# Kernel tuning notes

Hardware: AMD Instinct MI355X
Metric: run time of the kernel (lower is better)

Reference implementation:

```python
import jax, jax.numpy as jnp
import numpy as np

N, C, EMB_ROWS = 524288, 128, 32
SLOPE = 0.2  # leaky_relu negative slope


def setup_inputs() -> dict:
    key = jax.random.key(0)
    k1, k2, k3, k4, k5 = jax.random.split(key, 5)
    x = jax.random.normal(k1, (N, C), jnp.float32)
    perm = jax.random.permutation(k2, N)  # fixed stand-in for torch.randperm
    depth = jax.random.normal(k3, (EMB_ROWS, 128), jnp.float32)  # Embedding(32,128), N(0,1) init
    fan_in = 2 * C * 2
    bound = 1.0 / np.sqrt(fan_in)
    W = jax.random.uniform(k4, (C, 2 * C, 2), jnp.float32, -bound, bound)  # Conv1d weight (O,I,K)
    b = jax.random.uniform(k5, (C,), jnp.float32, -bound, bound)
    return {"x": x, "depth": depth, "W": W, "b": b, "perm": perm}


def reference(x, depth, W, b, perm):
    c = W.shape[0]
    x = x[perm]                      # random shuffle of rows
    x = x.T.reshape(1, c, -1)        # [1, C, N]
    i = 0
    # Python while over STATIC shapes -> unrolled at trace time (~log2(N) steps)
    while x.shape[-1] > 1:
        L = x.shape[-1]
        e = jnp.broadcast_to(depth[i].reshape(1, 128, 1), (1, 128, L))
        x = jnp.concatenate([x, e], axis=1)   # [1, 2C, L]
        x = jax.lax.conv_general_dilated(
            x, W, window_strides=(1,), padding="VALID",
            dimension_numbers=("NCH", "OIH", "NCH"))  # [1, C, L-1]
        x = x + b.reshape(1, -1, 1)
        x = jnp.where(x >= 0, x, SLOPE * x)   # leaky_relu(0.2)
        if x.shape[-1] == 1:
            break
        # MaxPool1d(2,2): floor(L/2), drops trailing element for odd L
        x = jax.lax.reduce_window(
            x, -jnp.inf, jax.lax.max,
            window_dimensions=(1, 1, 2), window_strides=(1, 1, 2),
            padding="VALID")
        i += 1
    return x.reshape(c, 1).T  # [1, C]
```

## Files before the change

kernel.cpp:

```cpp
#include <hip/hip_runtime.h>
#include <hip/hip_bf16.h>


typedef __bf16 v8bf __attribute__((ext_vector_type(8)));
typedef float v16f __attribute__((ext_vector_type(16)));

__device__ __forceinline__ ushort f2bf(float f) {
    __hip_bfloat16 h = __float2bfloat16(f);
    return *reinterpret_cast<ushort*>(&h);
}
__device__ __forceinline__ unsigned pack2(float lo, float hi) {
    return (unsigned)f2bf(lo) | ((unsigned)f2bf(hi) << 16);
}
__device__ __forceinline__ float leaky(float y) { return (y >= 0.f) ? y : 0.2f * y; }

#define ZACC {0.f,0.f,0.f,0.f,0.f,0.f,0.f,0.f,0.f,0.f,0.f,0.f,0.f,0.f,0.f,0.f}

__global__ void bias_kernel(const float* __restrict__ W, const float* __restrict__ b,
                            const float* __restrict__ depth, float* __restrict__ Bst) {
    int i = blockIdx.x, o = threadIdx.x;
    const float* Wo = W + (size_t)o * 512 + 256;
    const float* di = depth + (size_t)i * 128;
    float s = b[o];
#pragma unroll 8
    for (int c = 0; c < 128; ++c) s += di[c] * (Wo[2 * c] + Wo[2 * c + 1]);
    Bst[i * 128 + o] = s;
}

__global__ void repack_kernel(const float* __restrict__ W, ushort* __restrict__ A) {
    int o = blockIdx.x, c = threadIdx.x;
    float v = (c < 128) ? W[(size_t)o * 512 + 2 * c] : W[(size_t)o * 512 + 2 * (c - 128) + 1];
    A[o * 256 + c] = f2bf(v);
}

#define WAVE_SETUP()                                                          \
    const int tid = threadIdx.x;                                              \
    const int lane = tid & 63;                                                \
    const int w = tid >> 6;                                                   \
    const int n31 = lane & 31;                                                \
    const int h = lane >> 5;                                                  \
    v8bf af[16];                                                              \
    {                                                                         \
        const ushort* Arow = A + (size_t)(w * 32 + n31) * 256 + h * 8;        \
        _Pragma("unroll")                                                     \
        for (int s = 0; s < 16; ++s) af[s] = *(const v8bf*)&Arow[s * 16];     \
    }

#define LOAD_BIAS(dst_, Bs)                                                   \
    float dst_[16];                                                           \
    _Pragma("unroll")                                                         \
    for (int r = 0; r < 16; ++r)                                              \
        dst_[r] = (Bs)[w * 32 + (r & 3) + 8 * (r >> 2) + 4 * h];

#define MFMA_TILE_LDS(buf, r0_, r1_, acc)                                     \
    {                                                                         \
        const ushort* sp0 = (buf) + (r0_) * 128;                              \
        const ushort* sp1 = (buf) + (r1_) * 128;                              \
        const int mm0 = (r0_) & 15, mm1 = (r1_) & 15;                         \
        _Pragma("unroll")                                                     \
        for (int s = 0; s < 8; ++s)                                           \
            acc = __builtin_amdgcn_mfma_f32_32x32x16_bf16(                    \
                af[s], *(const v8bf*)&sp0[((2 * s + h) ^ mm0) * 8], acc, 0, 0, 0); \
        _Pragma("unroll")                                                     \
        for (int s = 0; s < 8; ++s)                                           \
            acc = __builtin_amdgcn_mfma_f32_32x32x16_bf16(                    \
                af[8 + s], *(const v8bf*)&sp1[((2 * s + h) ^ mm1) * 8], acc, 0, 0, 0); \
    }

__global__ __launch_bounds__(256)
void pair_fused(const ushort* __restrict__ Xin,
                const float* __restrict__ x0,
                const int* __restrict__ perm,
                const ushort* __restrict__ A,
                const float* __restrict__ Bst2,
                ushort* __restrict__ Y,
                int Lin, int Lp2, int stage0) {
    __shared__ __align__(16) ushort xin[132 * 128];
    __shared__ __align__(16) ushort mid[65 * 128];
    __shared__ int prow[132];

    const int U = blockIdx.x * 32;
    const int t0 = U * 4;

    if (stage0) {
        for (int r = threadIdx.x; r < 132; r += 256)
            prow[r] = perm[min(t0 + r, Lin - 1)];
        __syncthreads();
    }
    for (int idx = threadIdx.x; idx < 132 * 16; idx += 256) {
        int row = idx >> 4, ck = idx & 15;
        int t = min(t0 + row, Lin - 1);
        int dst = row * 128 + ((ck ^ (row & 15)) * 8);
        if (stage0) {
            const float* s = x0 + (size_t)prow[row] * 128 + ck * 8;
            float4 a = *(const float4*)s;
            float4 bq = *(const float4*)(s + 4);
            uint4 v;
            v.x = pack2(a.x, a.y);  v.y = pack2(a.z, a.w);
            v.z = pack2(bq.x, bq.y); v.w = pack2(bq.z, bq.w);
            *(uint4*)&xin[dst] = v;
        } else {
            *(uint4*)&xin[dst] = *(const uint4*)&Xin[(size_t)t * 128 + ck * 8];
        }
    }
    __syncthreads();

    WAVE_SETUP();

    {
        LOAD_BIAS(bias_r, Bst2);
#pragma unroll
        for (int ti = 0; ti < 5; ++ti) {
            const int p = 32 * ti + n31;
            const int r0 = min(p, 131), r1 = min(p + 1, 131);
            v16f acc = ZACC;
            MFMA_TILE_LDS(xin, r0, r1, acc);
            const int u1 = 16 * ti + (n31 >> 1);
            const bool act = !(lane & 1) && (u1 < 65);
#pragma unroll
            for (int q = 0; q < 4; ++q) {
                float pv[4];
#pragma unroll
                for (int j = 0; j < 4; ++j) {
                    float y = leaky(acc[4 * q + j] + bias_r[4 * q + j]);
                    float y2 = __shfl_xor(y, 1, 64);
                    pv[j] = fmaxf(y, y2);
                }
                if (act) {
                    uint2 v;
                    v.x = pack2(pv[0], pv[1]);
                    v.y = pack2(pv[2], pv[3]);
                    *(uint2*)&mid[u1 * 128 + (((4 * w + q) ^ (u1 & 15)) * 8) + 4 * h] = v;
                }
            }
        }
    }
    __syncthreads();

    {
        LOAD_BIAS(bias_r, Bst2 + 128);
#pragma unroll
        for (int ti = 0; ti < 2; ++ti) {
            const int p = 32 * ti + n31;
            v16f acc = ZACC;
            MFMA_TILE_LDS(mid, p, p + 1, acc);
            const int u2 = U + 16 * ti + (n31 >> 1);
            const bool act = !(lane & 1) && (u2 < Lp2);
#pragma unroll
            for (int q = 0; q < 4; ++q) {
                float pv[4];
#pragma unroll
                for (int j = 0; j < 4; ++j) {
                    float y = leaky(acc[4 * q + j] + bias_r[4 * q + j]);
                    float y2 = __shfl_xor(y, 1, 64);
                    pv[j] = fmaxf(y, y2);
                }
                if (act) {
                    uint2 v;
                    v.x = pack2(pv[0], pv[1]);
                    v.y = pack2(pv[2], pv[3]);
                    *(uint2*)&Y[(size_t)u2 * 128 + w * 32 + 8 * q + 4 * h] = v;
                }
            }
        }
    }
}

__global__ __launch_bounds__(256)
void tail_fused(const ushort* __restrict__ Xg, const ushort* __restrict__ A,
                const float* __restrict__ BstAll, float* __restrict__ out) {
    extern __shared__ __align__(16) ushort tbuf[];
    ushort* buf0 = tbuf;
    ushort* buf1 = tbuf + 255 * 128;

    WAVE_SETUP();

    int Lin = 511;
    for (int st = 0; st < 8; ++st) {
        const int Lp = (Lin - 1) >> 1;
        LOAD_BIAS(bias_r, BstAll + (size_t)(10 + st) * 128);
        ushort* dst = (st & 1) ? buf1 : buf0;
        const ushort* src = (st & 1) ? buf0 : buf1;
        const int ntiles = (Lin - 1 + 31) >> 5;
        for (int ti = 0; ti < ntiles; ++ti) {
            const int t = ti * 32 + n31;
            const int r0 = min(t, Lin - 1), r1 = min(t + 1, Lin - 1);
            v16f acc = ZACC;
            if (st == 0) {
                const ushort* p0 = Xg + (size_t)r0 * 128 + h * 8;
                const ushort* p1 = Xg + (size_t)r1 * 128 + h * 8;
#pragma unroll
                for (int s = 0; s < 8; ++s)
                    acc = __builtin_amdgcn_mfma_f32_32x32x16_bf16(
                        af[s], *(const v8bf*)&p0[s * 16], acc, 0, 0, 0);
#pragma unroll
                for (int s = 0; s < 8; ++s)
                    acc = __builtin_amdgcn_mfma_f32_32x32x16_bf16(
                        af[8 + s], *(const v8bf*)&p1[s * 16], acc, 0, 0, 0);
            } else {
                MFMA_TILE_LDS(src, r0, r1, acc);
            }
            const int u = t >> 1;
            const bool act = !(lane & 1) && (u < Lp);
#pragma unroll
            for (int q = 0; q < 4; ++q) {
                float pv[4];
#pragma unroll
                for (int j = 0; j < 4; ++j) {
                    float y = leaky(acc[4 * q + j] + bias_r[4 * q + j]);
                    float y2 = __shfl_xor(y, 1, 64);
                    pv[j] = fmaxf(y, y2);
                }
                if (act) {
                    if (st < 7) {
                        uint2 v;
                        v.x = pack2(pv[0], pv[1]);
                        v.y = pack2(pv[2], pv[3]);
                        *(uint2*)&dst[u * 128 + (((4 * w + q) ^ (u & 15)) * 8) + 4 * h] = v;
                    } else {
                        float4 o = {pv[0], pv[1], pv[2], pv[3]};
                        *(float4*)&out[w * 32 + 8 * q + 4 * h] = o;
                    }
                }
            }
        }
        __syncthreads();
        Lin = Lp;
    }
}

extern "C" void kernel_launch(void* const* d_in, const int* in_sizes, int n_in,
                              void* d_out, int out_size, void* d_ws, size_t ws_size,
                              hipStream_t stream) {
    const float* x     = (const float*)d_in[0];
    const float* depth = (const float*)d_in[1];
    const float* W     = (const float*)d_in[2];
    const float* b     = (const float*)d_in[3];
    const int*   perm  = (const int*)d_in[4];
    float* out = (float*)d_out;

    char* ws = (char*)d_ws;
    float*  Bst = (float*)ws;
    ushort* A   = (ushort*)(ws + 16384);
    ushort* R0  = (ushort*)(ws + 16384 + 65536);
    ushort* R1  = (ushort*)(ws + 16384 + 65536 + (size_t)131071 * 256);

    bias_kernel<<<18, 128, 0, stream>>>(W, b, depth, Bst);
    repack_kernel<<<128, 256, 0, stream>>>(W, A);

    pair_fused<<<4096, 256, 0, stream>>>(nullptr, x, perm, A, Bst, R0,
                                         524288, 131071, 1);
    pair_fused<<<1024, 256, 0, stream>>>(R0, nullptr, nullptr, A, Bst + 2 * 128, R1,
                                         131071, 32767, 0);
    pair_fused<<<256, 256, 0, stream>>>(R1, nullptr, nullptr, A, Bst + 4 * 128, R0,
                                        32767, 8191, 0);
    pair_fused<<<64, 256, 0, stream>>>(R0, nullptr, nullptr, A, Bst + 6 * 128, R1,
                                       8191, 2047, 0);
    pair_fused<<<16, 256, 0, stream>>>(R1, nullptr, nullptr, A, Bst + 8 * 128, R0,
                                       2047, 511, 0);
    tail_fused<<<1, 256, (255 + 127) * 128 * 2, stream>>>(R0, A, Bst, out);
}
```

Baseline: 556.2 us.

## Split MFMA accumulator chains, raise wave priority, batch gather loads

Result: slower. 572.5 us (+2.9%).

```diff
diff --git a/kernel.cpp b/kernel.cpp
--- a/kernel.cpp
+++ b/kernel.cpp
@@ -57,14 +57,17 @@
         const ushort* sp0 = (buf) + (r0_) * 128;                              \
         const ushort* sp1 = (buf) + (r1_) * 128;                              \
         const int mm0 = (r0_) & 15, mm1 = (r1_) & 15;                         \
+        v16f accB_ = ZACC;                                                    \
+        __builtin_amdgcn_s_setprio(1);                                        \
         _Pragma("unroll")                                                     \
-        for (int s = 0; s < 8; ++s)                                           \
+        for (int s = 0; s < 8; ++s) {                                         \
             acc = __builtin_amdgcn_mfma_f32_32x32x16_bf16(                    \
                 af[s], *(const v8bf*)&sp0[((2 * s + h) ^ mm0) * 8], acc, 0, 0, 0); \
-        _Pragma("unroll")                                                     \
-        for (int s = 0; s < 8; ++s)                                           \
-            acc = __builtin_amdgcn_mfma_f32_32x32x16_bf16(                    \
-                af[8 + s], *(const v8bf*)&sp1[((2 * s + h) ^ mm1) * 8], acc, 0, 0, 0); \
+            accB_ = __builtin_amdgcn_mfma_f32_32x32x16_bf16(                  \
+                af[8 + s], *(const v8bf*)&sp1[((2 * s + h) ^ mm1) * 8], accB_, 0, 0, 0); \
+        }                                                                     \
+        __builtin_amdgcn_s_setprio(0);                                        \
+        acc += accB_;                                                         \
     }
 
 __global__ __launch_bounds__(256)
@@ -77,30 +80,60 @@
                 int Lin, int Lp2, int stage0) {
     __shared__ __align__(16) ushort xin[132 * 128];
     __shared__ __align__(16) ushort mid[65 * 128];
-    __shared__ int prow[132];
 
     const int U = blockIdx.x * 32;
     const int t0 = U * 4;
 
     if (stage0) {
-        for (int r = threadIdx.x; r < 132; r += 256)
-            prow[r] = perm[min(t0 + r, Lin - 1)];
-        __syncthreads();
-    }
-    for (int idx = threadIdx.x; idx < 132 * 16; idx += 256) {
-        int row = idx >> 4, ck = idx & 15;
-        int t = min(t0 + row, Lin - 1);
-        int dst = row * 128 + ((ck ^ (row & 15)) * 8);
-        if (stage0) {
-            const float* s = x0 + (size_t)prow[row] * 128 + ck * 8;
-            float4 a = *(const float4*)s;
-            float4 bq = *(const float4*)(s + 4);
-            uint4 v;
-            v.x = pack2(a.x, a.y);  v.y = pack2(a.z, a.w);
-            v.z = pack2(bq.x, bq.y); v.w = pack2(bq.z, bq.w);
-            *(uint4*)&xin[dst] = v;
-        } else {
-            *(uint4*)&xin[dst] = *(const uint4*)&Xin[(size_t)t * 128 + ck * 8];
+        int pr[9];
+        float4 aa[9], bb[9];
+#pragma unroll
+        for (int k = 0; k < 9; ++k) {
+            int idx = threadIdx.x + 256 * k;
+            if (idx < 132 * 16) {
+                int row = idx >> 4;
+                pr[k] = perm[min(t0 + row, Lin - 1)];
+            }
+        }
+#pragma unroll
+        for (int k = 0; k < 9; ++k) {
+            int idx = threadIdx.x + 256 * k;
+            if (idx < 132 * 16) {
+                int ck = idx & 15;
+                const float* s = x0 + (size_t)pr[k] * 128 + ck * 8;
+                aa[k] = *(const float4*)s;
+                bb[k] = *(const float4*)(s + 4);
+            }
+        }
+#pragma unroll
+        for (int k = 0; k < 9; ++k) {
+            int idx = threadIdx.x + 256 * k;
+            if (idx < 132 * 16) {
+                int row = idx >> 4, ck = idx & 15;
+                uint4 v;
+                v.x = pack2(aa[k].x, aa[k].y);  v.y = pack2(aa[k].z, aa[k].w);
+                v.z = pack2(bb[k].x, bb[k].y);  v.w = pack2(bb[k].z, bb[k].w);
+                *(uint4*)&xin[row * 128 + ((ck ^ (row & 15)) * 8)] = v;
+            }
+        }
+    } else {
+        uint4 vv[9];
+#pragma unroll
+        for (int k = 0; k < 9; ++k) {
+            int idx = threadIdx.x + 256 * k;
+            if (idx < 132 * 16) {
+                int row = idx >> 4, ck = idx & 15;
+                int t = min(t0 + row, Lin - 1);
+                vv[k] = *(const uint4*)&Xin[(size_t)t * 128 + ck * 8];
+            }
+        }
+#pragma unroll
+        for (int k = 0; k < 9; ++k) {
+            int idx = threadIdx.x + 256 * k;
+            if (idx < 132 * 16) {
+                int row = idx >> 4, ck = idx & 15;
+                *(uint4*)&xin[row * 128 + ((ck ^ (row & 15)) * 8)] = vv[k];
+            }
         }
     }
     __syncthreads();
@@ -189,14 +222,17 @@
             if (st == 0) {
                 const ushort* p0 = Xg + (size_t)r0 * 128 + h * 8;
                 const ushort* p1 = Xg + (size_t)r1 * 128 + h * 8;
-#pragma unroll
-                for (int s = 0; s < 8; ++s)
+                v16f accB = ZACC;
+                __builtin_amdgcn_s_setprio(1);
+#pragma unroll
+                for (int s = 0; s < 8; ++s) {
                     acc = __builtin_amdgcn_mfma_f32_32x32x16_bf16(
                         af[s], *(const v8bf*)&p0[s * 16], acc, 0, 0, 0);
-#pragma unroll
-                for (int s = 0; s < 8; ++s)
-                    acc = __builtin_amdgcn_mfma_f32_32x32x16_bf16(
-                        af[8 + s], *(const v8bf*)&p1[s * 16], acc, 0, 0, 0);
+                    accB = __builtin_amdgcn_mfma_f32_32x32x16_bf16(
+                        af[8 + s], *(const v8bf*)&p1[s * 16], accB, 0, 0, 0);
+                }
+                __builtin_amdgcn_s_setprio(0);
+                acc += accB;
             } else {
                 MFMA_TILE_LDS(src, r0, r1, acc);
             }
```
